# Kernel optimization log

Hardware: AMD Instinct MI355X
Metric: run time of the kernel (lower is better)

## Reference

```python
import jax, jax.numpy as jnp
import numpy as np

B, N, DIM, H = 4, 16384, 384, 8
C = DIM // H          # head_dim = 48
M = C // 2            # kernel_ratio=0.5 -> m = 24
EPS = 1e-6

def setup_inputs() -> dict:
    key = jax.random.key(0)
    k0, k1, k2, k3, k4 = jax.random.split(key, 5)
    x = jax.random.normal(k0, (B, N, DIM), jnp.float32)
    # small init scale keeps exp() in the kernel feature map well-conditioned
    qkv_w = jax.random.normal(k1, (3 * DIM, DIM), jnp.float32) * 0.02
    proj_w = jax.random.normal(k2, (DIM, DIM), jnp.float32) * 0.02
    proj_b = jax.random.normal(k3, (DIM,), jnp.float32) * 0.02
    # per-head orthogonal random features (rows orthonormal), scaled by sqrt(m)
    g = jax.random.normal(k4, (H, C, M), jnp.float32)
    q_mat, _ = jnp.linalg.qr(g)                  # (H, C, M), orthonormal columns
    w = jnp.transpose(q_mat, (0, 2, 1)) * np.sqrt(M)  # (H, M, C)
    return {"x": x, "qkv_w": qkv_w, "proj_w": proj_w, "proj_b": proj_b, "w": w}

def _feature_map(t, w, scale):
    # t: [B,H,N,C], w: [H,M,C]
    t = t * scale
    logits = jnp.einsum('bhnc,hmc->bhnm', t, w) - 0.5 * jnp.sum(t * t, axis=-1, keepdims=True)
    return jnp.exp(logits) / np.sqrt(w.shape[1])

def reference(x, qkv_w, proj_w, proj_b, w):
    b, n, dim = x.shape
    h, m, c = w.shape
    scale = c ** (-0.25)
    # qkv projection, split into q,k,v with layout (qkv H C)
    qkv = (x @ qkv_w.T).reshape(b, n, 3, h, c).transpose(2, 0, 3, 1, 4)  # [3,B,H,N,C]
    q, k, v = qkv[0], qkv[1], qkv[2]
    phi_q = _feature_map(q, w, scale)   # [B,H,N,M]
    phi_k = _feature_map(k, w, scale)   # [B,H,N,M]
    # normalizer: q . sum_n(k)
    D = jnp.einsum('bhnm,bhm->bhn', phi_q, phi_k.sum(axis=2)) + EPS  # [B,H,N]
    # linear-attention state: K^T V, then Q @ (K^T V)
    ktv = jnp.einsum('bhnm,bhnc->bhmc', phi_k, v)                    # [B,H,M,C]
    out = jnp.einsum('bhnm,bhmc->bhnc', phi_q, ktv) / D[..., None]   # [B,H,N,C]
    out = out.transpose(0, 2, 1, 3).reshape(b, n, dim)               # [B,N,dim]
    return out @ proj_w.T + proj_b
```

## Files before the change

### kernel.cpp

```cpp
#include <hip/hip_runtime.h>
#include <hip/hip_bf16.h>

typedef __bf16 bf16x8 __attribute__((ext_vector_type(8)));
typedef float  f32x4  __attribute__((ext_vector_type(4)));
typedef short  short8 __attribute__((ext_vector_type(8)));
typedef float  f32x4v __attribute__((ext_vector_type(4)));

#define B_SZ 4
#define N_SZ 16384
#define DIM_SZ 384
#define H_SZ 8
#define C_SZ 48
#define M_SZ 24

static constexpr float SCALE = 0.37991784282579627f;
static constexpr float RSM   = 0.20412414523193154f;
static constexpr float EPS_V = 1e-6f;


__device__ __forceinline__ void gld_lds16(void* lds, const void* g) {
  __builtin_amdgcn_global_load_lds(
      (const __attribute__((address_space(1))) unsigned int*)g,
      (__attribute__((address_space(3))) unsigned int*)lds, 16, 0, 0);
}

__device__ __forceinline__ float bf2f(short s) {
  union { unsigned u; float f; } cv;
  cv.u = ((unsigned)(unsigned short)s) << 16;
  return cv.f;
}
__device__ __forceinline__ short f2bf_s(float f) {
  const __bf16 b = (__bf16)f;
  return __builtin_bit_cast(short, b);
}
__device__ __forceinline__ f32x4 MF(bf16x8 a, bf16x8 b, f32x4 c) {
  return __builtin_amdgcn_mfma_f32_16x16x32_bf16(a, b, c, 0, 0, 0);
}

__global__ __launch_bounds__(256, 2) void gemmxa(
    const float* __restrict__ Af, const __bf16* __restrict__ Bm,
    __bf16* __restrict__ Cout, int Nw, int K) {
  extern __shared__ __align__(16) char lds[];
  const int t    = threadIdx.x;
  const int lane = t & 63;
  const int wid  = t >> 6;
  const int wm   = wid >> 1;
  const int wn   = wid & 1;
  const int l15  = lane & 15;
  const int kgq  = lane >> 4;

  const int gx   = gridDim.x;
  const int nwg  = gx * gridDim.y;
  const int orig = blockIdx.y * gx + blockIdx.x;
  const int qq   = nwg >> 3, rr = nwg & 7;
  const int xcd  = orig & 7, pos = orig >> 3;
  const int id   = (xcd < rr ? xcd*(qq+1) : rr*(qq+1) + (xcd-rr)*qq) + pos;
  const int row0 = (id / gx) * 128, col0 = (id % gx) * 128;

  const int nt = K >> 6;
  const int sg = (t & 7) ^ ((t >> 3) & 7);

  f32x4v areg[4][2];
  auto loadA = [&](int kt) {
    const size_t kofs = (size_t)kt * 64 + (t & 7) * 8;
    #pragma unroll
    for (int i = 0; i < 4; ++i) {
      const int r = i*32 + (t >> 3);
      const float* src = Af + (size_t)(row0 + r) * K + kofs;
      areg[i][0] = *(const f32x4v*)(src);
      areg[i][1] = *(const f32x4v*)(src + 4);
    }
  };
  auto writeA = [&](int kt) {
    char* buf = lds + (kt & 1) * 32768;
    #pragma unroll
    for (int i = 0; i < 4; ++i) {
      const int r = i*32 + (t >> 3);
      short8 pk;
      #pragma unroll
      for (int j = 0; j < 4; ++j) {
        pk[j]     = f2bf_s(areg[i][0][j]);
        pk[4 + j] = f2bf_s(areg[i][1][j]);
      }
      *(short8*)(buf + r*128 + (((t & 7) * 16) ^ ((r & 7) << 4))) = pk;
    }
  };
  auto stageB = [&](int kt) {
    char* buf = lds + (kt & 1) * 32768 + 16384;
    const size_t kofs = (size_t)kt * 64 + sg * 8;
    #pragma unroll
    for (int i = 0; i < 4; ++i) {
      const int r = i*32 + (t >> 3);
      gld_lds16(buf + i*4096 + t*16, Bm + (size_t)(col0 + r) * K + kofs);
    }
  };

  f32x4 acc[4][4] = {};
  loadA(0); stageB(0);

  for (int kt = 0; kt < nt; ++kt) {
    asm volatile("s_waitcnt vmcnt(0)" ::: "memory");
    writeA(kt);
    asm volatile("s_waitcnt lgkmcnt(0)" ::: "memory");
    __builtin_amdgcn_s_barrier();
    __builtin_amdgcn_sched_barrier(0);

    char* buf = lds + (kt & 1) * 32768;
    if (kt + 1 < nt) { loadA(kt + 1); stageB(kt + 1); }

    bf16x8 bfr[4][2];
    #pragma unroll
    for (int ni = 0; ni < 4; ++ni) {
      const int brow = wn*64 + ni*16 + l15;
      #pragma unroll
      for (int kk = 0; kk < 2; ++kk)
        bfr[ni][kk] = *(const bf16x8*)(buf + 16384 + brow*128
                          + ((kk*64 + kgq*16) ^ ((brow & 7) << 4)));
    }
    #pragma unroll
    for (int mi = 0; mi < 4; ++mi) {
      const int arow = wm*64 + mi*16 + l15;
      const bf16x8 a0 = *(const bf16x8*)(buf + arow*128
                          + ((kgq*16)      ^ ((arow & 7) << 4)));
      const bf16x8 a1 = *(const bf16x8*)(buf + arow*128
                          + ((64 + kgq*16) ^ ((arow & 7) << 4)));
      __builtin_amdgcn_s_setprio(1);
      #pragma unroll
      for (int ni = 0; ni < 4; ++ni) {
        acc[mi][ni] = MF(a0, bfr[ni][0], acc[mi][ni]);
        acc[mi][ni] = MF(a1, bfr[ni][1], acc[mi][ni]);
      }
      __builtin_amdgcn_s_setprio(0);
    }
  }

  const int cr = (lane >> 4) << 2;
  #pragma unroll
  for (int mi = 0; mi < 4; ++mi) {
    #pragma unroll
    for (int ni = 0; ni < 4; ++ni) {
      const int col = col0 + wn*64 + ni*16 + l15;
      #pragma unroll
      for (int j = 0; j < 4; ++j) {
        const int row = row0 + wm*64 + mi*16 + cr + j;
        Cout[(size_t)row * Nw + col] = (__bf16)acc[mi][ni][j];
      }
    }
  }
}

template<int EPI>
__global__ __launch_bounds__(256, 2) void gemm2b(
    const __bf16* __restrict__ A, const __bf16* __restrict__ Bm,
    void* __restrict__ Cout, const float* __restrict__ bias,
    int M, int Nw, int K,
    size_t aSlice, size_t bSlice, size_t cSlice) {
  extern __shared__ __align__(16) char lds[];
  const int t    = threadIdx.x;
  const int lane = t & 63;
  const int wid  = t >> 6;
  const int wm   = wid >> 1;
  const int wn   = wid & 1;
  const int l15  = lane & 15;
  const int kgq  = lane >> 4;

  const int bz = blockIdx.z;
  const __bf16* Ab = A  + (size_t)bz * aSlice;
  const __bf16* Bb = Bm + (size_t)bz * bSlice;

  const int gx   = gridDim.x;
  const int nwg  = gx * gridDim.y;
  const int orig = blockIdx.y * gx + blockIdx.x;
  const int qq   = nwg >> 3, rr = nwg & 7;
  const int xcd  = orig & 7, pos = orig >> 3;
  const int id   = (xcd < rr ? xcd*(qq+1) : rr*(qq+1) + (xcd-rr)*qq) + pos;
  const int row0 = (id / gx) * 128, col0 = (id % gx) * 128;

  const int nt = K >> 6;
  const int sg = (t & 7) ^ ((t >> 3) & 7);

  auto stage = [&](int kt) {
    char* buf = lds + (kt & 1) * 32768;
    const size_t kofs = (size_t)kt * 64 + sg * 8;
    #pragma unroll
    for (int i = 0; i < 4; ++i) {
      const int r = i*32 + (t >> 3);
      gld_lds16(buf + i*4096 + t*16,         Ab + (size_t)(row0 + r) * K + kofs);
      gld_lds16(buf + 16384 + i*4096 + t*16, Bb + (size_t)(col0 + r) * K + kofs);
    }
  };

  f32x4 acc[4][4] = {};
  stage(0);

  for (int kt = 0; kt < nt; ++kt) {
    asm volatile("s_waitcnt vmcnt(0)" ::: "memory");
    __builtin_amdgcn_s_barrier();
    __builtin_amdgcn_sched_barrier(0);

    char* buf = lds + (kt & 1) * 32768;
    if (kt + 1 < nt) stage(kt + 1);

    bf16x8 bfr[4][2];
    #pragma unroll
    for (int ni = 0; ni < 4; ++ni) {
      const int brow = wn*64 + ni*16 + l15;
      #pragma unroll
      for (int kk = 0; kk < 2; ++kk)
        bfr[ni][kk] = *(const bf16x8*)(buf + 16384 + brow*128
                          + ((kk*64 + kgq*16) ^ ((brow & 7) << 4)));
    }
    #pragma unroll
    for (int mi = 0; mi < 4; ++mi) {
      const int arow = wm*64 + mi*16 + l15;
      const bf16x8 a0 = *(const bf16x8*)(buf + arow*128
                          + ((kgq*16)      ^ ((arow & 7) << 4)));
      const bf16x8 a1 = *(const bf16x8*)(buf + arow*128
                          + ((64 + kgq*16) ^ ((arow & 7) << 4)));
      __builtin_amdgcn_s_setprio(1);
      #pragma unroll
      for (int ni = 0; ni < 4; ++ni) {
        acc[mi][ni] = MF(a0, bfr[ni][0], acc[mi][ni]);
        acc[mi][ni] = MF(a1, bfr[ni][1], acc[mi][ni]);
      }
      __builtin_amdgcn_s_setprio(0);
    }
  }

  const int cr = (lane >> 4) << 2;
  #pragma unroll
  for (int mi = 0; mi < 4; ++mi) {
    #pragma unroll
    for (int ni = 0; ni < 4; ++ni) {
      const int col = col0 + wn*64 + ni*16 + l15;
      #pragma unroll
      for (int j = 0; j < 4; ++j) {
        const int row = row0 + wm*64 + mi*16 + cr + j;
        const float v = acc[mi][ni][j];
        if (EPI == 1) {
          ((float*)Cout + (size_t)bz*cSlice)[(size_t)row * Nw + col] = v + bias[col];
        } else {
          ((__bf16*)Cout + (size_t)bz*cSlice)[(size_t)row * Nw + col] = (__bf16)v;
        }
      }
    }
  }
}

__global__ __launch_bounds__(256) void prep_kernel(
    const float* __restrict__ qkv_w, const float* __restrict__ w,
    __bf16* __restrict__ Baug) {
  const int bid = blockIdx.x, t = threadIdx.x;
  if (bid < 144) {
    const int i = bid * 256 + t;
    const float* src = qkv_w + (size_t)384 * 384;
    const f32x4v a = *(const f32x4v*)(src + (size_t)i*8);
    const f32x4v c = *(const f32x4v*)(src + (size_t)i*8 + 4);
    short8 pk;
    #pragma unroll
    for (int j = 0; j < 4; ++j) {
      pk[j]     = f2bf_s(a[j]);
      pk[4 + j] = f2bf_s(c[j]);
    }
    *(short8*)(Baug + (size_t)i*8) = pk;
  } else {
    const int idx = (bid - 144) * 256 + t;
    const int d = idx % 384, rs = idx / 384;
    const int side = rs / 192, hm = rs % 192;
    const int h = hm / 24;
    const float* wr = w + (size_t)hm * 48;
    const float* qw = qkv_w + ((size_t)(side*384 + h*48)) * 384 + d;
    float acc = 0.f;
    #pragma unroll
    for (int c = 0; c < 48; ++c)
      acc += wr[c] * qw[(size_t)c * 384];
    Baug[(size_t)(768 + side*192 + hm) * 384 + d] = (__bf16)(acc * SCALE);
  }
}

__global__ __launch_bounds__(256) void ktv_fused(
    const __bf16* __restrict__ kvll, float* __restrict__ ktv_part) {
  const int b = blockIdx.z, h = blockIdx.y, sp = blockIdx.x;
  const int t = threadIdx.x, wv = t >> 6, lane = t & 63;
  const int l15 = lane & 15, g = lane >> 4;
  const int bh = b*H_SZ + h;

  __shared__ __align__(16) char smem[47616];
  __bf16 (*vT)[48][40]  = (__bf16(*)[48][40])(smem);
  __bf16 (*phiT)[24][40]= (__bf16(*)[24][40])(smem + 15360);
  __bf16 (*kS)[32][56]  = (__bf16(*)[32][56])(smem + 23040);
  __bf16 (*lkS)[32][40] = (__bf16(*)[32][40])(smem + 37376);
  float  (*red)[1184]   = (float(*)[1184])(smem);

  f32x4 acc[2][3] = {};
  f32x4 aks[2] = {};
  const int nbase = sp*256 + wv*64;

  bf16x8 ones{};
  if (l15 == 0)
    #pragma unroll
    for (int j = 0; j < 8; ++j) ones[j] = (__bf16)1.0f;

  for (int step = 0; step < 2; ++step) {
    const int n0 = nbase + step*32;
    const __bf16* base = kvll + ((size_t)(b*N_SZ) + n0) * 1152;
    #pragma unroll
    for (int it = 0; it < 3; ++it) {
      const int task = it*64 + lane;
      const int tk = task / 6, p = task % 6;
      const short8 r = *(const short8*)(base + (size_t)tk*1152 + 384 + h*C_SZ + p*8);
      #pragma unroll
      for (int e = 0; e < 8; ++e)
        vT[wv][p*8 + e][tk] = __builtin_bit_cast(__bf16, (short)r[e]);
    }
    #pragma unroll
    for (int it = 0; it < 3; ++it) {
      const int task = it*64 + lane;
      const int tk = task / 6, p = task % 6;
      const short8 r = *(const short8*)(base + (size_t)tk*1152 + h*C_SZ + p*8);
      *(short8*)(&kS[wv][tk][p*8]) = r;
    }
    {
      {
        const int tk = lane / 3, p = lane % 3;
        const short8 r = *(const short8*)(base + (size_t)tk*1152 + 960 + h*24 + p*8);
        *(short8*)(&lkS[wv][tk][p*8]) = r;
      }
      if (lane < 32) {
        const int task = 64 + lane;
        const int tk = task / 3, p = task % 3;
        const short8 r = *(const short8*)(base + (size_t)tk*1152 + 960 + h*24 + p*8);
        *(short8*)(&lkS[wv][tk][p*8]) = r;
      }
    }
    if (lane < 32) {
      float ss = 0.f;
      #pragma unroll
      for (int i = 0; i < 6; ++i) {
        const short8 r = *(const short8*)(&kS[wv][lane][i*8]);
        #pragma unroll
        for (int j = 0; j < 8; ++j) { const float f = bf2f(r[j]) * SCALE; ss += f*f; }
      }
      const float hs = 0.5f * ss;
      #pragma unroll
      for (int i = 0; i < 3; ++i) {
        const short8 r = *(const short8*)(&lkS[wv][lane][i*8]);
        #pragma unroll
        for (int j = 0; j < 8; ++j)
          phiT[wv][i*8 + j][lane] = (__bf16)(__expf(bf2f(r[j]) - hs) * RSM);
      }
    }
    const bf16x8 a0 = *(const bf16x8*)(&phiT[wv][l15][g*8]);
    bf16x8 a1{};
    if (l15 < 8) a1 = *(const bf16x8*)(&phiT[wv][16 + l15][g*8]);
    #pragma unroll
    for (int ct = 0; ct < 3; ++ct) {
      const bf16x8 bfr = *(const bf16x8*)(&vT[wv][ct*16 + l15][g*8]);
      acc[0][ct] = MF(a0, bfr, acc[0][ct]);
      acc[1][ct] = MF(a1, bfr, acc[1][ct]);
    }
    aks[0] = MF(a0, ones, aks[0]);
    aks[1] = MF(a1, ones, aks[1]);
  }

  __syncthreads();

  #pragma unroll
  for (int mt = 0; mt < 2; ++mt)
    #pragma unroll
    for (int ct = 0; ct < 3; ++ct)
      #pragma unroll
      for (int jj = 0; jj < 4; ++jj) {
        const int row = mt*16 + g*4 + jj;
        if (row < 24)
          red[wv][row*48 + ct*16 + l15] = acc[mt][ct][jj];
      }
  if (l15 == 0) {
    #pragma unroll
    for (int mt = 0; mt < 2; ++mt)
      #pragma unroll
      for (int jj = 0; jj < 4; ++jj) {
        const int m = mt*16 + g*4 + jj;
        if (m < 24) red[wv][1152 + m] = aks[mt][jj];
      }
  }
  __syncthreads();
  float* outp = ktv_part + ((size_t)bh*64 + sp) * 1184;
  for (int i = t; i < 1176; i += 256)
    outp[i] = red[0][i] + red[1][i] + red[2][i] + red[3][i];
}

__global__ __launch_bounds__(256) void reduce_ktv(
    const float* __restrict__ ktv_part, float* __restrict__ ktv_f,
    float* __restrict__ ksum) {
  const int bh = blockIdx.x >> 2, q = blockIdx.x & 3;
  const int i0 = q * 296;
  const int iend = (i0 + 296 < 1176) ? i0 + 296 : 1176;
  for (int i = i0 + threadIdx.x; i < iend; i += 256) {
    float s = 0.f;
    #pragma unroll 8
    for (int sp = 0; sp < 64; ++sp)
      s += ktv_part[((size_t)bh*64 + sp) * 1184 + i];
    if (i < 1152) ktv_f[bh*1152 + i] = s;
    else          ksum[bh*24 + (i - 1152)] = s;
  }
}

__global__ __launch_bounds__(256) void gtpp_kernel(
    const float* __restrict__ ktv_f, const float* __restrict__ proj_w,
    const __bf16* __restrict__ kvll, const float* __restrict__ ksum,
    __bf16* __restrict__ Gt, __bf16* __restrict__ Pp) {
  const int bid = blockIdx.x, t = threadIdx.x;
  if (bid < 1152) {
    const int idx = bid * 256 + t;
    const int hm = idx % 192, o = (idx / 192) % 384, b = idx / (192*384);
    const int h = hm / 24, m = hm % 24;
    const float* kt = ktv_f + ((size_t)(b*H_SZ + h))*1152 + m*48;
    const float* pw = proj_w + (size_t)o*384 + h*48;
    float acc = 0.f;
    #pragma unroll
    for (int c = 0; c < 48; ++c) acc += kt[c] * pw[c];
    Gt[((size_t)b*384 + o)*192 + hm] = (__bf16)acc;
    return;
  }
  const int blk = bid - 1152;
  const int tok = blk * 256 + t;
  const int b = (blk * 256) >> 14;
  __shared__ float ksl[192];
  if (t < 192) ksl[t] = ksum[b*192 + t];
  __syncthreads();

  const __bf16* lq = kvll + (size_t)tok*1152 + 768;
  __bf16* po = Pp + (size_t)tok*192;
  #pragma unroll
  for (int h = 0; h < 8; ++h) {
    float ph[24];
    float d = EPS_V;
    #pragma unroll
    for (int i = 0; i < 3; ++i) {
      const short8 r = *(const short8*)(lq + h*24 + i*8);
      #pragma unroll
      for (int j = 0; j < 8; ++j) {
        const float p = __expf(bf2f(r[j])) * RSM;
        ph[i*8 + j] = p;
        d += p * ksl[h*24 + i*8 + j];
      }
    }
    const float inv = 1.0f / d;
    #pragma unroll
    for (int i = 0; i < 3; ++i) {
      short8 pk;
      #pragma unroll
      for (int j = 0; j < 8; ++j) pk[j] = f2bf_s(ph[i*8 + j] * inv);
      *(short8*)(po + h*24 + i*8) = pk;
    }
  }
}

extern "C" void kernel_launch(void* const* d_in, const int* in_sizes, int n_in,
                              void* d_out, int out_size, void* d_ws, size_t ws_size,
                              hipStream_t stream) {
  (void)in_sizes; (void)n_in; (void)out_size; (void)ws_size;
  const float* x      = (const float*)d_in[0];
  const float* qkv_w  = (const float*)d_in[1];
  const float* proj_w = (const float*)d_in[2];
  const float* proj_b = (const float*)d_in[3];
  const float* w      = (const float*)d_in[4];
  float* out = (float*)d_out;

  const size_t BN_TOT = (size_t)B_SZ * N_SZ;
  char* ws = (char*)d_ws;
  size_t off = 0;
  auto alloc = [&](size_t bytes) {
    char* p = ws + off;
    off += (bytes + 255) & ~(size_t)255;
    return p;
  };
  __bf16* Baug     = (__bf16*)alloc((size_t)1152 * 384 * 2);
  __bf16* kvll     = (__bf16*)alloc(BN_TOT * 1152 * 2);
  float*  ktv_part = (float*)alloc((size_t)32 * 64 * 1184 * 4);
  float*  ktv_f    = (float*)alloc((size_t)32 * 1152 * 4);
  float*  ksum     = (float*)alloc((size_t)32 * 24 * 4);
  __bf16* Pp       = (__bf16*)alloc(BN_TOT * 192 * 2);
  __bf16* Gt       = (__bf16*)alloc((size_t)B_SZ * 384 * 192 * 2);

  static const int LDS2B = 2 * 32768;
  hipFuncSetAttribute(reinterpret_cast<const void*>(&gemmxa),
                      hipFuncAttributeMaxDynamicSharedMemorySize, LDS2B);
  hipFuncSetAttribute(reinterpret_cast<const void*>(&gemm2b<1>),
                      hipFuncAttributeMaxDynamicSharedMemorySize, LDS2B);

  prep_kernel<<<720, 256, 0, stream>>>(qkv_w, w, Baug);

  gemmxa<<<dim3(1152/128, BN_TOT/128), 256, LDS2B, stream>>>(
      x, Baug, kvll, 1152, DIM_SZ);

  ktv_fused<<<dim3(64, H_SZ, B_SZ), 256, 0, stream>>>(kvll, ktv_part);
  reduce_ktv<<<128, 256, 0, stream>>>(ktv_part, ktv_f, ksum);

  gtpp_kernel<<<1408, 256, 0, stream>>>(ktv_f, proj_w, kvll, ksum, Gt, Pp);

  gemm2b<1><<<dim3(384/128, N_SZ/128, B_SZ), 256, LDS2B, stream>>>(
      Pp, Gt, out, proj_b, N_SZ, 384, 192,
      (size_t)N_SZ * 192, (size_t)384 * 192, (size_t)N_SZ * 384);
}
```

Measured before the change: 216.3 us.

## Pre-convert x to bf16 and use async LDS staging with 128x64 tiles

The fp32-to-bf16 conversion of x moves out of the QKV GEMM into the prep kernel, which writes a bf16 copy of x to workspace. The GEMM can then stage both A and B straight into LDS with global_load_lds and drop the register round-trip and convert step. The tile shrinks from 128x128 to 128x64 and occupancy goes from 2 to 3 blocks. In exchange, x makes an extra pass through HBM (read fp32, write bf16, read bf16), and the A tile is reloaded once per column tile.

```diff
diff --git a/kernel.cpp b/kernel.cpp
--- a/kernel.cpp
+++ b/kernel.cpp
@@ -37,8 +37,8 @@
   return __builtin_amdgcn_mfma_f32_16x16x32_bf16(a, b, c, 0, 0, 0);
 }
 
-__global__ __launch_bounds__(256, 2) void gemmxa(
-    const float* __restrict__ Af, const __bf16* __restrict__ Bm,
+__global__ __launch_bounds__(256, 3) void gemm2c(
+    const __bf16* __restrict__ A, const __bf16* __restrict__ Bm,
     __bf16* __restrict__ Cout, int Nw, int K) {
   extern __shared__ __align__(16) char lds[];
   const int t    = threadIdx.x;
@@ -55,63 +55,41 @@
   const int qq   = nwg >> 3, rr = nwg & 7;
   const int xcd  = orig & 7, pos = orig >> 3;
   const int id   = (xcd < rr ? xcd*(qq+1) : rr*(qq+1) + (xcd-rr)*qq) + pos;
-  const int row0 = (id / gx) * 128, col0 = (id % gx) * 128;
+  const int row0 = (id / gx) * 128, col0 = (id % gx) * 64;
 
   const int nt = K >> 6;
   const int sg = (t & 7) ^ ((t >> 3) & 7);
 
-  f32x4v areg[4][2];
-  auto loadA = [&](int kt) {
-    const size_t kofs = (size_t)kt * 64 + (t & 7) * 8;
+  auto stage = [&](int kt) {
+    char* buf = lds + (kt & 1) * 24576;
+    const size_t kofs = (size_t)kt * 64 + sg * 8;
     #pragma unroll
     for (int i = 0; i < 4; ++i) {
       const int r = i*32 + (t >> 3);
-      const float* src = Af + (size_t)(row0 + r) * K + kofs;
-      areg[i][0] = *(const f32x4v*)(src);
-      areg[i][1] = *(const f32x4v*)(src + 4);
+      gld_lds16(buf + i*4096 + t*16, A + (size_t)(row0 + r) * K + kofs);
+    }
+    #pragma unroll
+    for (int i = 0; i < 2; ++i) {
+      const int r = i*32 + (t >> 3);
+      gld_lds16(buf + 16384 + i*4096 + t*16, Bm + (size_t)(col0 + r) * K + kofs);
     }
   };
-  auto writeA = [&](int kt) {
-    char* buf = lds + (kt & 1) * 32768;
-    #pragma unroll
-    for (int i = 0; i < 4; ++i) {
-      const int r = i*32 + (t >> 3);
-      short8 pk;
-      #pragma unroll
-      for (int j = 0; j < 4; ++j) {
-        pk[j]     = f2bf_s(areg[i][0][j]);
-        pk[4 + j] = f2bf_s(areg[i][1][j]);
-      }
-      *(short8*)(buf + r*128 + (((t & 7) * 16) ^ ((r & 7) << 4))) = pk;
-    }
-  };
-  auto stageB = [&](int kt) {
-    char* buf = lds + (kt & 1) * 32768 + 16384;
-    const size_t kofs = (size_t)kt * 64 + sg * 8;
-    #pragma unroll
-    for (int i = 0; i < 4; ++i) {
-      const int r = i*32 + (t >> 3);
-      gld_lds16(buf + i*4096 + t*16, Bm + (size_t)(col0 + r) * K + kofs);
-    }
-  };
-
-  f32x4 acc[4][4] = {};
-  loadA(0); stageB(0);
+
+  f32x4 acc[4][2] = {};
+  stage(0);
 
   for (int kt = 0; kt < nt; ++kt) {
     asm volatile("s_waitcnt vmcnt(0)" ::: "memory");
-    writeA(kt);
-    asm volatile("s_waitcnt lgkmcnt(0)" ::: "memory");
     __builtin_amdgcn_s_barrier();
     __builtin_amdgcn_sched_barrier(0);
 
-    char* buf = lds + (kt & 1) * 32768;
-    if (kt + 1 < nt) { loadA(kt + 1); stageB(kt + 1); }
-
-    bf16x8 bfr[4][2];
-    #pragma unroll
-    for (int ni = 0; ni < 4; ++ni) {
-      const int brow = wn*64 + ni*16 + l15;
+    char* buf = lds + (kt & 1) * 24576;
+    if (kt + 1 < nt) stage(kt + 1);
+
+    bf16x8 bfr[2][2];
+    #pragma unroll
+    for (int ni = 0; ni < 2; ++ni) {
+      const int brow = wn*32 + ni*16 + l15;
       #pragma unroll
       for (int kk = 0; kk < 2; ++kk)
         bfr[ni][kk] = *(const bf16x8*)(buf + 16384 + brow*128
@@ -126,7 +104,7 @@
                           + ((64 + kgq*16) ^ ((arow & 7) << 4)));
       __builtin_amdgcn_s_setprio(1);
       #pragma unroll
-      for (int ni = 0; ni < 4; ++ni) {
+      for (int ni = 0; ni < 2; ++ni) {
         acc[mi][ni] = MF(a0, bfr[ni][0], acc[mi][ni]);
         acc[mi][ni] = MF(a1, bfr[ni][1], acc[mi][ni]);
       }
@@ -138,8 +116,8 @@
   #pragma unroll
   for (int mi = 0; mi < 4; ++mi) {
     #pragma unroll
-    for (int ni = 0; ni < 4; ++ni) {
-      const int col = col0 + wn*64 + ni*16 + l15;
+    for (int ni = 0; ni < 2; ++ni) {
+      const int col = col0 + wn*32 + ni*16 + l15;
       #pragma unroll
       for (int j = 0; j < 4; ++j) {
         const int row = row0 + wm*64 + mi*16 + cr + j;
@@ -248,11 +226,23 @@
 }
 
 __global__ __launch_bounds__(256) void prep_kernel(
-    const float* __restrict__ qkv_w, const float* __restrict__ w,
+    const float* __restrict__ x, const float* __restrict__ qkv_w,
+    const float* __restrict__ w, __bf16* __restrict__ x_bf,
     __bf16* __restrict__ Baug) {
   const int bid = blockIdx.x, t = threadIdx.x;
-  if (bid < 144) {
+  if (bid < 12288) {
     const int i = bid * 256 + t;
+    const f32x4v a = *(const f32x4v*)(x + (size_t)i*8);
+    const f32x4v c = *(const f32x4v*)(x + (size_t)i*8 + 4);
+    short8 pk;
+    #pragma unroll
+    for (int j = 0; j < 4; ++j) {
+      pk[j]     = f2bf_s(a[j]);
+      pk[4 + j] = f2bf_s(c[j]);
+    }
+    *(short8*)(x_bf + (size_t)i*8) = pk;
+  } else if (bid < 12432) {
+    const int i = (bid - 12288) * 256 + t;
     const float* src = qkv_w + (size_t)384 * 384;
     const f32x4v a = *(const f32x4v*)(src + (size_t)i*8);
     const f32x4v c = *(const f32x4v*)(src + (size_t)i*8 + 4);
@@ -264,7 +254,7 @@
     }
     *(short8*)(Baug + (size_t)i*8) = pk;
   } else {
-    const int idx = (bid - 144) * 256 + t;
+    const int idx = (bid - 12432) * 256 + t;
     const int d = idx % 384, rs = idx / 384;
     const int side = rs / 192, hm = rs % 192;
     const int h = hm / 24;
@@ -476,6 +466,7 @@
     off += (bytes + 255) & ~(size_t)255;
     return p;
   };
+  __bf16* x_bf     = (__bf16*)alloc(BN_TOT * DIM_SZ * 2);
   __bf16* Baug     = (__bf16*)alloc((size_t)1152 * 384 * 2);
   __bf16* kvll     = (__bf16*)alloc(BN_TOT * 1152 * 2);
   float*  ktv_part = (float*)alloc((size_t)32 * 64 * 1184 * 4);
@@ -484,16 +475,17 @@
   __bf16* Pp       = (__bf16*)alloc(BN_TOT * 192 * 2);
   __bf16* Gt       = (__bf16*)alloc((size_t)B_SZ * 384 * 192 * 2);
 
+  static const int LDS2C = 2 * 24576;
   static const int LDS2B = 2 * 32768;
-  hipFuncSetAttribute(reinterpret_cast<const void*>(&gemmxa),
-                      hipFuncAttributeMaxDynamicSharedMemorySize, LDS2B);
+  hipFuncSetAttribute(reinterpret_cast<const void*>(&gemm2c),
+                      hipFuncAttributeMaxDynamicSharedMemorySize, LDS2C);
   hipFuncSetAttribute(reinterpret_cast<const void*>(&gemm2b<1>),
                       hipFuncAttributeMaxDynamicSharedMemorySize, LDS2B);
 
-  prep_kernel<<<720, 256, 0, stream>>>(qkv_w, w, Baug);
-
-  gemmxa<<<dim3(1152/128, BN_TOT/128), 256, LDS2B, stream>>>(
-      x, Baug, kvll, 1152, DIM_SZ);
+  prep_kernel<<<13008, 256, 0, stream>>>(x, qkv_w, w, x_bf, Baug);
+
+  gemm2c<<<dim3(1152/64, BN_TOT/128), 256, LDS2C, stream>>>(
+      x_bf, Baug, kvll, 1152, DIM_SZ);
 
   ktv_fused<<<dim3(64, H_SZ, B_SZ), 256, 0, stream>>>(kvll, ktv_part);
   reduce_ktv<<<128, 256, 0, stream>>>(ktv_part, ktv_f, ksum);
```

Result: faster. 198.7 us (-8.1%).
